# Performance work log

Hardware: AMD Instinct MI355X
Metric: run time of the kernel (lower is better)

The kernel has to match this reference:

```python
import jax, jax.numpy as jnp
import numpy as np
from jax import lax

T, B, CIN, H, W = 16, 8, 16, 64, 64
HID = (32, 32)
K = 3


def _conv(x, w):
    # x: [B, C, H, W], w: [O, I, K, K], SAME padding, stride 1
    return lax.conv_general_dilated(
        x, w, window_strides=(1, 1), padding='SAME',
        dimension_numbers=('NCHW', 'OIHW', 'NCHW'))


def _run_layer(x_seq, w, b):
    # x_seq: [T, B, Cin_l, H, W]; w: [4*hid, Cin_l+hid, K, K]; b: [4*hid]
    hid = w.shape[0] // 4
    bsz = x_seq.shape[1]
    h0 = jnp.zeros((bsz, hid, H, W), x_seq.dtype)
    c0 = jnp.zeros_like(h0)

    def step(carry, xt):
        h, c = carry
        gates = _conv(jnp.concatenate([xt, h], axis=1), w) + b[None, :, None, None]
        i, f, o, g = jnp.split(gates, 4, axis=1)
        c_new = jax.nn.sigmoid(f) * c + jax.nn.sigmoid(i) * jnp.tanh(g)
        h_new = jax.nn.sigmoid(o) * jnp.tanh(c_new)
        return (h_new, c_new), h_new

    (h_T, c_T), h_seq = lax.scan(step, (h0, c0), x_seq)
    return h_seq, h_T, c_T


def setup_inputs() -> dict:
    key = jax.random.key(0)
    ks = jax.random.split(key, 5)
    x = jax.random.normal(ks[0], (T, B, CIN, H, W), dtype=jnp.float32)
    s0 = 1.0 / np.sqrt((CIN + HID[0]) * K * K)
    s1 = 1.0 / np.sqrt((HID[0] + HID[1]) * K * K)
    W0 = jax.random.normal(ks[1], (4 * HID[0], CIN + HID[0], K, K), dtype=jnp.float32) * s0
    b0 = jax.random.normal(ks[2], (4 * HID[0],), dtype=jnp.float32) * s0
    W1 = jax.random.normal(ks[3], (4 * HID[1], HID[0] + HID[1], K, K), dtype=jnp.float32) * s1
    b1 = jax.random.normal(ks[4], (4 * HID[1],), dtype=jnp.float32) * s1
    return {"x": x, "W0": W0, "b0": b0, "W1": W1, "b1": b1}


def reference(x, W0, b0, W1, b1):
    h_seq0, h0_T, c0_T = _run_layer(x, W0, b0)
    h_seq1, h1_T, c1_T = _run_layer(h_seq0, W1, b1)
    # return_all_layers=True: per-layer hidden sequences + per-layer final (h, c)
    return (h_seq0, h_seq1, h0_T, c0_T, h1_T, c1_T)
```

## Files before the change

kernel.cpp:

```cpp
#include <hip/hip_runtime.h>
#include <math.h>

#define TT   16
#define BATCH 8
#define HH   64
#define WW   64
#define HWSZ 4096
#define HID  32
#define CT_STRIDE 68

typedef __bf16 bf16x8 __attribute__((ext_vector_type(8)));
typedef float  f32x4  __attribute__((ext_vector_type(4)));
typedef unsigned short u16;
typedef unsigned int   u32;
typedef unsigned long long u64;
typedef u32 u32x4 __attribute__((ext_vector_type(4)));

__device__ __forceinline__ u16 f2bf(float f) {
    union { float f; u32 u; } v; v.f = f;
    u32 r = v.u + 0x7FFF + ((v.u >> 16) & 1);
    return (u16)(r >> 16);
}

__device__ __forceinline__ int cidx(int row, int p) {
    return row * CT_STRIDE + (p ^ ((row & 3) << 2));
}

__device__ __forceinline__ void gl2lds(const void* g, void* l) {
    __builtin_amdgcn_global_load_lds(
        (const __attribute__((address_space(1))) u32*)g,
        (__attribute__((address_space(3))) u32*)l, 16, 0, 0);
}

__device__ __forceinline__ void prep_wp(const float* __restrict__ W,
                                        u16* __restrict__ wf, int cinl, int idx) {
    const int lane = idx & 63, nt = (idx >> 6) & 7, g = idx >> 9;
    const int cho = nt * 16 + (lane & 15);
    const int k0  = g * 32 + (lane >> 4) * 8;
    u16 o[8];
#pragma unroll
    for (int j = 0; j < 8; ++j) {
        const int k = k0 + j;
        const int tap = k / cinl;
        const int cin = k - tap * cinl;
        o[j] = (tap < 9) ? f2bf(W[((size_t)cho * cinl + cin) * 9 + tap]) : (u16)0;
    }
    ((uint4*)wf)[idx] = *(uint4*)&o[0];
}

__global__ __launch_bounds__(256)
void prep_all(const float* __restrict__ x, u16* __restrict__ xbf,
              const float* __restrict__ W0, u16* __restrict__ wf0,
              const float* __restrict__ W1, u16* __restrict__ wf1) {
    const int bid = blockIdx.x, tid = threadIdx.x;
    if (bid < 2048) {
        const int p = bid * 256 + tid;
        const int tb = p >> 12, pix = p & 4095;
        const float* src = x + ((size_t)tb * 16) * HWSZ + pix;
        u16 o[16];
#pragma unroll
        for (int c = 0; c < 16; ++c) o[c] = f2bf(src[(size_t)c * HWSZ]);
        uint4* dst = (uint4*)(xbf + (size_t)p * 16);
        dst[0] = *(uint4*)&o[0];
        dst[1] = *(uint4*)&o[8];
    } else if (bid < 2076) {
        prep_wp(W0, wf0, 48, (bid - 2048) * 256 + tid);
    } else if (bid < 2112) {
        prep_wp(W1, wf1, 64, (bid - 2076) * 256 + tid);
    }
}

template<int NG, int CINL, int XCH>
__device__ __forceinline__ void conv_step(
    const u16* __restrict__ srcX,
    const u16* __restrict__ srcH,
    const uint4* __restrict__ wf,
    const float* __restrict__ bias,
    float* __restrict__ cbuf,
    float* __restrict__ hout, float* __restrict__ hT,
    u16* __restrict__ hbfo, const u16* __restrict__ zp,
    int t0, int blk, uint4* lds4, float* ctile)
{
    const int tid = threadIdx.x;
    const int y0 = (blk & 31) * 2;
    const int b  = blk >> 5;
    const int lane = tid & 63;
    const int w    = tid >> 6;

    for (int j = w; j < 33; j += 4) {
        const int q  = j * 64 + lane;
        const int pr = q >> 3;
        const int px = pr % 66;
        const int r  = pr / 66;
        const int c8log = (q & 7) ^ (px & 7);
        const int gy = y0 - 1 + r;
        const int gx = px - 1;
        const int pix = b * HWSZ + gy * WW + gx;
        const int cin8 = c8log * 8;
        const bool inb = (gy >= 0) && (gy < HH) && (gx >= 0) && (gx < WW);
        const u16* s =
            (cin8 < XCH) ? (srcX + (size_t)pix * XCH + cin8)
          : (cin8 < XCH + 32) ? (t0 ? zp : (srcH + (size_t)pix * 32 + (cin8 - XCH)))
          : zp;
        if (!inb) s = zp;
        gl2lds(s, (void*)(lds4 + j * 64));
    }

    const int fr  = tid >> 2;
    const int fyy = fr >> 5, fc = fr & 31;
    const size_t gflat = ((size_t)(b * HID + fc) * HH + (y0 + fyy)) * WW;
    if (!t0) {
#pragma unroll
        for (int j = 0; j < 4; ++j) {
            const int q = j * 4 + (tid & 3);
            *(uint4*)(ctile + cidx(fr, q * 4)) =
                *(const uint4*)(cbuf + gflat + q * 4);
        }
    }
    __syncthreads();

    const int l15   = lane & 15, lhi = lane >> 4;
    const int khalf = w & 1;
    const int wrow  = w >> 1;

    float bv[4];
#pragma unroll
    for (int n = 0; n < 4; ++n) bv[n] = bias[n * 32 + khalf * 16 + l15];
    f32x4 acc[4][4];
#pragma unroll
    for (int m = 0; m < 4; ++m)
#pragma unroll
        for (int n = 0; n < 4; ++n)
            acc[m][n] = (f32x4){bv[n], bv[n], bv[n], bv[n]};

    const int p0 = l15 + 1;

    auto LOADA = [&](bf16x8* dst, int g) {
        const int k0 = g * 32 + lhi * 8;
        int tap = k0 / CINL;  if (tap > 8) tap = 8;
        const int c8log = (k0 - tap * CINL) >> 3;
        const int ty = tap / 3;
        const int dx = tap - ty * 3 - 1;
        const int sr = wrow + ty;
#pragma unroll
        for (int m = 0; m < 4; ++m) {
            const int pxt = p0 + m * 16 + dx;
            dst[m] = __builtin_bit_cast(bf16x8,
                     lds4[(((sr * 66 + pxt) * 8) + c8log) ^ (pxt & 7)]);
        }
    };
    auto LOADB = [&](bf16x8* dst, int g) {
#pragma unroll
        for (int n = 0; n < 4; ++n)
            dst[n] = __builtin_bit_cast(bf16x8,
                     wf[((size_t)g * 8 + (khalf + 2 * n)) * 64 + lane]);
    };
    auto MFMAG = [&](const bf16x8* a, const bf16x8* bw) {
        __builtin_amdgcn_s_setprio(1);
#pragma unroll
        for (int n = 0; n < 4; ++n)
#pragma unroll
            for (int m = 0; m < 4; ++m)
                acc[m][n] = __builtin_amdgcn_mfma_f32_16x16x32_bf16(
                                a[m], bw[n], acc[m][n], 0, 0, 0);
        __builtin_amdgcn_s_setprio(0);
    };

    bf16x8 a0[4], a1[4], a2[4], b0[4], b1[4], b2[4];
    LOADB(b0, 0); LOADA(a0, 0);
    LOADB(b1, 1); LOADA(a1, 1);
    LOADB(b2, 2); LOADA(a2, 2);
#pragma unroll
    for (int g = 0; g < NG; g += 3) {
        MFMAG(a0, b0);
        if (g + 3 < NG) { LOADB(b0, g + 3); LOADA(a0, g + 3); }
        if (g + 1 < NG) {
            MFMAG(a1, b1);
            if (g + 4 < NG) { LOADB(b1, g + 4); LOADA(a1, g + 4); }
        }
        if (g + 2 < NG) {
            MFMAG(a2, b2);
            if (g + 5 < NG) { LOADB(b2, g + 5); LOADA(a2, g + 5); }
        }
    }

    __syncthreads();
    float* htile = (float*)lds4;

    const int c = khalf * 16 + l15;
    const int row = wrow * 32 + c;
#pragma unroll
    for (int m = 0; m < 4; ++m) {
#pragma unroll
        for (int rr = 0; rr < 4; ++rr) {
            const int p = m * 16 + lhi * 4 + rr;
            const int ci = cidx(row, p);
            const float cp = t0 ? 0.f : ctile[ci];
            const float iv = acc[m][0][rr], fv = acc[m][1][rr];
            const float ov = acc[m][2][rr], gv = acc[m][3][rr];
            const float ig = __builtin_amdgcn_rcpf(1.f + __expf(-iv));
            const float fg = __builtin_amdgcn_rcpf(1.f + __expf(-fv));
            const float og = __builtin_amdgcn_rcpf(1.f + __expf(-ov));
            const float gg = 1.f - 2.f * __builtin_amdgcn_rcpf(1.f + __expf(2.f * gv));
            const float cn = fg * cp + ig * gg;
            const float hn = og * (1.f - 2.f * __builtin_amdgcn_rcpf(1.f + __expf(2.f * cn)));
            ctile[ci] = cn;
            htile[ci] = hn;
        }
    }
    __syncthreads();

#pragma unroll
    for (int j = 0; j < 4; ++j) {
        const int q = j * 4 + (tid & 3);
        const int ci = cidx(fr, q * 4);
        const u32x4 hv = *(const u32x4*)(htile + ci);
        const uint4 cv = *(const uint4*)(ctile + ci);
        __builtin_nontemporal_store(hv, (u32x4*)(hout + gflat + q * 4));
        *(uint4*)(cbuf + gflat + q * 4) = cv;
        if (hT) __builtin_nontemporal_store(hv, (u32x4*)(hT + gflat + q * 4));
    }

#pragma unroll
    for (int j = 0; j < 4; ++j) {
        const int idx = j * 256 + tid;
        const int c4  = idx & 7;
        const int pxx = (idx >> 3) & 63;
        const int yy  = idx >> 9;
        u16 pk[4];
#pragma unroll
        for (int k = 0; k < 4; ++k)
            pk[k] = f2bf(htile[cidx(yy * 32 + c4 * 4 + k, pxx)]);
        const int pix = b * HWSZ + (y0 + yy) * WW + pxx;
        *(u64*)(hbfo + (size_t)pix * 32 + c4 * 4) = *(u64*)pk;
    }
}

__global__ __launch_bounds__(256, 2)
void fused_step(
    const u16* srcX0, const u16* srcH0, const uint4* wf0, const float* bias0,
    float* cbuf0, float* hout0, float* hT0, u16* hbfo0, int t00, int act0,
    const u16* srcX1, const u16* srcH1, const uint4* wf1, const float* bias1,
    float* cbuf1, float* hout1, float* hT1, u16* hbfo1, int t01, int act1,
    const u16* zp)
{
    __shared__ uint4 lds4[2112];
    __shared__ float ctile[64 * CT_STRIDE];
    const int blk = blockIdx.x;
    if (blk < 256) {
        if (!act0) return;
        conv_step<14, 48, 16>(srcX0, srcH0, wf0, bias0, cbuf0, hout0, hT0, hbfo0, zp, t00, blk, lds4, ctile);
    } else {
        if (!act1) return;
        conv_step<18, 64, 32>(srcX1, srcH1, wf1, bias1, cbuf1, hout1, hT1, hbfo1, zp, t01, blk - 256, lds4, ctile);
    }
}

extern "C" void kernel_launch(void* const* d_in, const int* in_sizes, int n_in,
                              void* d_out, int out_size, void* d_ws, size_t ws_size,
                              hipStream_t stream) {
    const float* x  = (const float*)d_in[0];
    const float* W0 = (const float*)d_in[1];
    const float* b0 = (const float*)d_in[2];
    const float* W1 = (const float*)d_in[3];
    const float* b1 = (const float*)d_in[4];
    float* out = (float*)d_out;

    float* hseq0 = out;
    float* hseq1 = out + 16777216;
    float* h0T   = out + 33554432;
    float* c0T   = out + 34603008;
    float* h1T   = out + 35651584;
    float* c1T   = out + 36700160;

    char* ws = (char*)d_ws;
    u16*  xbf = (u16*)ws;
    u16*  wf0 = (u16*)(ws + 16777216);
    u16*  wf1 = (u16*)(ws + 16777216 + 147456);
    u16*  hbf0[2] = { (u16*)(ws + 17072128), (u16*)(ws + 17072128 + 2097152) };
    u16*  hbf1[2] = { (u16*)(ws + 21266432), (u16*)(ws + 21266432 + 2097152) };
    u16*  zp = (u16*)(ws + 25460736);

    (void)hipMemsetAsync(zp, 0, 64, stream);
    prep_all<<<2112, 256, 0, stream>>>(x, xbf, W0, wf0, W1, wf1);

    const size_t hstep = (size_t)BATCH * HID * HWSZ;
    const size_t xstep = (size_t)BATCH * HWSZ * 16;

    for (int d = 0; d <= TT; ++d) {
        const int t0 = (d < TT) ? d : TT - 1;
        const int t1 = (d >= 1) ? d - 1 : 0;
        const int act0 = (d < TT), act1 = (d >= 1);
        fused_step<<<512, 256, 0, stream>>>(
            xbf + (size_t)t0 * xstep, hbf0[(t0 - 1) & 1],
            (const uint4*)wf0, b0, c0T,
            hseq0 + (size_t)t0 * hstep, (t0 == TT - 1 && act0) ? h0T : nullptr,
            hbf0[t0 & 1], (t0 == 0) ? 1 : 0, act0,
            hbf0[t1 & 1], hbf1[(t1 - 1) & 1],
            (const uint4*)wf1, b1, c1T,
            hseq1 + (size_t)t1 * hstep, (t1 == TT - 1 && act1) ? h1T : nullptr,
            hbf1[t1 & 1], (t1 == 0) ? 1 : 0, act1,
            zp);
    }
}
```

Baseline: 250.6 us.

## Stage conv weights through LDS in double-synced chunks instead of per-lane global loads

Weight fragments were previously read directly from global memory by every wave for each K-group. Now each block copies three K-groups of weights into a new 24 KB LDS buffer with async global-to-LDS loads, reads them into registers, and prefetches the next chunk while the MFMAs run. This is meant to cut redundant global/L2 weight traffic and latency in the MFMA loop. In exchange it adds two block barriers per chunk and extra LDS use, which could lower occupancy below the two blocks per CU the launch bounds ask for. It also masks the channel index in the A loads to stay inside the LDS tile.

```diff
diff --git a/kernel.cpp b/kernel.cpp
--- a/kernel.cpp
+++ b/kernel.cpp
@@ -79,8 +79,10 @@
     float* __restrict__ cbuf,
     float* __restrict__ hout, float* __restrict__ hT,
     u16* __restrict__ hbfo, const u16* __restrict__ zp,
-    int t0, int blk, uint4* lds4, float* ctile)
+    int t0, int blk, uint4* lds4, float* ctile, uint4* bbuf)
 {
+    constexpr int NT = (NG + 2) / 3;
+
     const int tid = threadIdx.x;
     const int y0 = (blk & 31) * 2;
     const int b  = blk >> 5;
@@ -106,6 +108,11 @@
         gl2lds(s, (void*)(lds4 + j * 64));
     }
 
+#pragma unroll
+    for (int jj = 0; jj < 6; ++jj)
+        gl2lds(wf + (size_t)(w * 6 + jj) * 64 + lane,
+               (void*)(bbuf + (w * 6 + jj) * 64));
+
     const int fr  = tid >> 2;
     const int fyy = fr >> 5, fc = fr & 31;
     const size_t gflat = ((size_t)(b * HID + fc) * HH + (y0 + fyy)) * WW;
@@ -138,7 +145,7 @@
     auto LOADA = [&](bf16x8* dst, int g) {
         const int k0 = g * 32 + lhi * 8;
         int tap = k0 / CINL;  if (tap > 8) tap = 8;
-        const int c8log = (k0 - tap * CINL) >> 3;
+        const int c8log = ((k0 - tap * CINL) >> 3) & 7;
         const int ty = tap / 3;
         const int dx = tap - ty * 3 - 1;
         const int sr = wrow + ty;
@@ -148,12 +155,6 @@
             dst[m] = __builtin_bit_cast(bf16x8,
                      lds4[(((sr * 66 + pxt) * 8) + c8log) ^ (pxt & 7)]);
         }
-    };
-    auto LOADB = [&](bf16x8* dst, int g) {
-#pragma unroll
-        for (int n = 0; n < 4; ++n)
-            dst[n] = __builtin_bit_cast(bf16x8,
-                     wf[((size_t)g * 8 + (khalf + 2 * n)) * 64 + lane]);
     };
     auto MFMAG = [&](const bf16x8* a, const bf16x8* bw) {
         __builtin_amdgcn_s_setprio(1);
@@ -166,25 +167,40 @@
         __builtin_amdgcn_s_setprio(0);
     };
 
-    bf16x8 a0[4], a1[4], a2[4], b0[4], b1[4], b2[4];
-    LOADB(b0, 0); LOADA(a0, 0);
-    LOADB(b1, 1); LOADA(a1, 1);
-    LOADB(b2, 2); LOADA(a2, 2);
-#pragma unroll
-    for (int g = 0; g < NG; g += 3) {
-        MFMAG(a0, b0);
-        if (g + 3 < NG) { LOADB(b0, g + 3); LOADA(a0, g + 3); }
-        if (g + 1 < NG) {
-            MFMAG(a1, b1);
-            if (g + 4 < NG) { LOADB(b1, g + 4); LOADA(a1, g + 4); }
-        }
-        if (g + 2 < NG) {
-            MFMAG(a2, b2);
-            if (g + 5 < NG) { LOADB(b2, g + 5); LOADA(a2, g + 5); }
-        }
-    }
-
-    __syncthreads();
+    bf16x8 a0[4], a1[4], a2[4];
+    LOADA(a0, 0); LOADA(a1, 1); LOADA(a2, 2);
+
+#pragma unroll
+    for (int T = 0; T < NT; ++T) {
+        bf16x8 br[3][4];
+#pragma unroll
+        for (int g3 = 0; g3 < 3; ++g3)
+#pragma unroll
+            for (int n = 0; n < 4; ++n)
+                br[g3][n] = __builtin_bit_cast(bf16x8,
+                            bbuf[((g3 * 8) + khalf + 2 * n) * 64 + lane]);
+        __syncthreads();
+
+        if (T + 1 < NT) {
+            const uint4* src = wf + (size_t)(T + 1) * 1536;
+#pragma unroll
+            for (int jj = 0; jj < 6; ++jj)
+                gl2lds(src + (size_t)(w * 6 + jj) * 64 + lane,
+                       (void*)(bbuf + (w * 6 + jj) * 64));
+        }
+
+#pragma unroll
+        for (int g3 = 0; g3 < 3; ++g3) {
+            const int g = T * 3 + g3;
+            if (g < NG) {
+                bf16x8* acur = (g % 3 == 0) ? a0 : (g % 3 == 1) ? a1 : a2;
+                MFMAG(acur, br[g3]);
+                if (g + 3 < NG) LOADA(acur, g + 3);
+            }
+        }
+        __syncthreads();
+    }
+
     float* htile = (float*)lds4;
 
     const int c = khalf * 16 + l15;
@@ -246,13 +262,14 @@
 {
     __shared__ uint4 lds4[2112];
     __shared__ float ctile[64 * CT_STRIDE];
+    __shared__ uint4 bbuf[1536];
     const int blk = blockIdx.x;
     if (blk < 256) {
         if (!act0) return;
-        conv_step<14, 48, 16>(srcX0, srcH0, wf0, bias0, cbuf0, hout0, hT0, hbfo0, zp, t00, blk, lds4, ctile);
+        conv_step<14, 48, 16>(srcX0, srcH0, wf0, bias0, cbuf0, hout0, hT0, hbfo0, zp, t00, blk, lds4, ctile, bbuf);
     } else {
         if (!act1) return;
-        conv_step<18, 64, 32>(srcX1, srcH1, wf1, bias1, cbuf1, hout1, hT1, hbfo1, zp, t01, blk - 256, lds4, ctile);
+        conv_step<18, 64, 32>(srcX1, srcH1, wf1, bias1, cbuf1, hout1, hT1, hbfo1, zp, t01, blk - 256, lds4, ctile, bbuf);
     }
 }
 
```

New measurement: 266.8 us. 6.4% more time.
